# Optimization experiments

Hardware: AMD Instinct MI355X
Metric: run time of the kernel (lower is better)

## Reference

```python
import jax, jax.numpy as jnp
import numpy as np

B_, L_, D_ = 2, 4096, 1024
E_ = 2
DI = E_ * D_            # 2048
H_ = 16
HD_ = DI // H_          # 128
N_ = 128
K_ = 4                  # d_conv
CS_ = 256               # SSD chunk size
MC_ = 256               # Hebbian memory chunk size
ALPHA = 0.5             # memory_alpha (== write_alpha default)


def _silu(x):
    return x * jax.nn.sigmoid(x)


def _rmsnorm(x, w, eps=1e-6):
    return x * jax.lax.rsqrt(jnp.mean(x * x, axis=-1, keepdims=True) + eps) * w


def setup_inputs() -> dict:
    key = jax.random.key(0)
    ks = jax.random.split(key, 8)
    proj_dim = 2 * DI + 2 * H_ * N_ + H_
    n = lambda k, sh, sc: jax.random.normal(k, sh, jnp.float32) * sc
    return {
        "x": n(ks[0], (B_, L_, D_), 1.0),
        "norm_w": jnp.ones((D_,), jnp.float32),
        "w_in": n(ks[1], (proj_dim, D_), 0.02),
        "conv_w": n(ks[2], (DI, K_), 0.2),
        "conv_b": jnp.zeros((DI,), jnp.float32),
        "A_log": jnp.log(2.0 * jnp.ones((H_,), jnp.float32)),
        "dt_bias": jnp.zeros((H_,), jnp.float32),
        "D_skip": jnp.ones((DI,), jnp.float32),
        "w_out": n(ks[3], (D_, DI), 0.02),
        "w_write": n(ks[4], (D_, D_), 0.02),
        "w_read": n(ks[5], (D_, D_), 0.02),
        "decay": jnp.float32(4.6),
    }


def _forward(x, norm_w, w_in, conv_w, conv_b, A_log, dt_bias, D_skip,
             w_out, w_write, w_read, decay):
    B, L, D = x.shape
    residual = x
    xn = _rmsnorm(x, norm_w)

    # ---- SSDBlock ----
    proj = xn @ w_in.T  # (B,L,2*DI+2*H*N+H)
    val = proj[..., :DI]
    gate = proj[..., DI:2 * DI]
    Bp = proj[..., 2 * DI:2 * DI + H_ * N_].reshape(B, L, H_, N_)
    Cp = proj[..., 2 * DI + H_ * N_:2 * DI + 2 * H_ * N_].reshape(B, L, H_, N_)
    dt = jax.nn.softplus(proj[..., -H_:] + dt_bias)  # (B,L,H)

    # causal depthwise conv1d (kernel K_, groups=DI)
    vp = jnp.pad(val, ((0, 0), (K_ - 1, 0), (0, 0)))
    val = sum(conv_w[:, k] * vp[:, k:k + L, :] for k in range(K_)) + conv_b
    val = _silu(val).reshape(B, L, H_, HD_)

    ld = dt * (-jnp.exp(A_log))  # log decay (B,L,H)

    nc = L // CS_
    to_chunks = lambda a: jnp.moveaxis(a.reshape(B, nc, CS_, *a.shape[2:]), 1, 0)
    tril = jnp.tril(jnp.ones((CS_, CS_), bool))
    Dv = D_skip.reshape(1, H_, 1, HD_)

    def ssd_chunk(h, inp):
        v_c, b_c, c_c, ld_c = inp  # (B,CS,H,HD), (B,CS,H,N), (B,CS,H,N), (B,CS,H)
        cum = jnp.cumsum(ld_c, axis=1)            # (B,CS,H)
        cum_h = jnp.transpose(cum, (0, 2, 1))     # (B,H,CS)
        dd = cum_h[:, :, :, None] - cum_h[:, :, None, :]
        Lmat = jnp.where(tril, jnp.exp(dd), 0.0)
        M = jnp.einsum('blhn,bmhn->bhlm', c_c, b_c) * Lmat
        v_h = jnp.transpose(v_c, (0, 2, 1, 3))    # (B,H,CS,HD)
        Y = M @ v_h
        Y = Y + jnp.einsum('blhn,bhdn,blh->bhld', c_c, h, jnp.exp(cum))
        Y = Y + Dv * v_h
        h = jnp.exp(cum[:, -1])[:, :, None, None] * h + \
            jnp.einsum('blhd,blhn,blh->bhdn', v_c, b_c, jnp.exp(cum[:, -1:, :] - cum))
        return h, Y

    h0 = jnp.zeros((B, H_, HD_, N_), jnp.float32)
    _, Ys = jax.lax.scan(ssd_chunk, h0,
                         (to_chunks(val), to_chunks(Bp), to_chunks(Cp), to_chunks(ld)))
    # (nc,B,H,CS,HD) -> (B,L,DI)
    Y = jnp.transpose(Ys, (1, 0, 3, 2, 4)).reshape(B, L, DI)
    out = (Y * _silu(gate)) @ w_out.T  # (B,L,D)

    # ---- Hebbian memory (chunkwise) ----
    gamma = jax.nn.sigmoid(decay)
    lg = jnp.log(gamma)
    v = out @ w_write.T
    wk = jnp.pad(out[:, :-1], ((0, 0), (1, 0), (0, 0)))  # shifted write keys
    p = jnp.arange(MC_)
    diffs = jnp.maximum(p[:, None] - 1 - p[None, :], 0).astype(jnp.float32)
    causal = (p[:, None] > p[None, :]).astype(jnp.float32)
    Mmem = jnp.exp(diffs * lg) * causal
    gp = gamma ** p                    # read decay by position in chunk
    gw = gamma ** (MC_ - 1 - p)        # write decay to end of chunk
    nm = L // MC_
    tom = lambda a: jnp.moveaxis(a.reshape(B, nm, MC_, D), 1, 0)

    def mem_chunk(W, inp):
        rk_c, wk_c, v_c = inp  # (B,MC,D)
        inter = jnp.einsum('bde,bte->btd', W, rk_c) * gp[None, :, None]
        S = jnp.einsum('bie,bje->bij', rk_c, wk_c)
        intra = (S * Mmem) @ v_c
        W = gamma ** MC_ * W + jnp.einsum('btd,bte->bde', v_c * gw[None, :, None], wk_c)
        return W, inter + intra

    W0 = jnp.zeros((B, D, D), jnp.float32)
    _, reads = jax.lax.scan(mem_chunk, W0, (tom(out), tom(wk), tom(v)))
    reads = jnp.moveaxis(reads, 0, 1).reshape(B, L, D)
    out = out + ALPHA * (reads @ w_read.T)
    return residual + out


def reference(x, norm_w, w_in, conv_w, conv_b, A_log, dt_bias, D_skip,
              w_out, w_write, w_read, decay):
    return _forward(x, norm_w, w_in, conv_w, conv_b, A_log, dt_bias, D_skip,
                    w_out, w_write, w_read, decay)
```

## Files before the change

### kernel.cpp

```cpp
#include <hip/hip_runtime.h>
#include <hip/hip_bf16.h>

typedef __hip_bfloat16 bf16;
typedef __attribute__((ext_vector_type(8))) short short8;
typedef __attribute__((ext_vector_type(4))) float floatx4;

#define B_ 2
#define L_ 4096
#define D_ 1024
#define DI_ 2048
#define H_ 16
#define HD_ 128
#define N_ 128
#define CS_ 256
#define MC_ 256
#define NC_ 16
#define PROJ_ 8208

__device__ __forceinline__ float bf2f(short s) {
    return __uint_as_float(((unsigned)(unsigned short)s) << 16);
}

__device__ __forceinline__ void gl_lds16(const void* g, void* s) {
    __builtin_amdgcn_global_load_lds(
        (const __attribute__((address_space(1))) void*)g,
        (__attribute__((address_space(3))) void*)s, 16, 0, 0);
}

struct GemmP {
    const bf16* A; const bf16* Bt;
    float* C; bf16* CB; bf16* CB2; bf16* CB3;
    const float* add0; const float* add1; const bf16* add0b; const float* scr;
    long lda, ldb, ldc;
    int M, N, K, zinner;
    long a_zo, a_zi, b_zo, b_zi, c_zo, c_zi;
};

template<int EPI>
__global__ __launch_bounds__(256, 2) void gemm_bt(GemmP p)
{
    int NT = gridDim.x, MT = gridDim.y;
    long T = (long)NT * MT * gridDim.z;
    long flat = ((long)blockIdx.z * MT + blockIdx.y) * NT + blockIdx.x;
    int xcd = (int)(flat & 7);
    long q = flat >> 3;
    long Tq = T >> 3; int Tr = (int)(T & 7);
    long tile = (long)xcd * Tq + (long)(xcd < Tr ? xcd : Tr) + q;
    long per_z = (long)NT * MT;
    int z = (int)(tile / per_z);
    int t2 = (int)(tile - (long)z * per_z);
    int FG = NT >> 3;
    int g, width, within;
    if (t2 < FG * MT * 8) { g = t2 / (MT * 8); width = 8; within = t2 - g * MT * 8; }
    else                  { g = FG; width = NT - FG * 8; within = t2 - FG * MT * 8; }
    int m_outer = within / (8 * width);
    int hb = MT - m_outer * 8; if (hb > 8) hb = 8;
    int inner = within - m_outer * 8 * width;
    int n_in = inner / hb, m_in = inner - n_in * hb;
    int m0 = (m_outer * 8 + m_in) * 128;
    int n0 = (g * 8 + n_in) * 128;

    int zo = z / p.zinner, zi = z % p.zinner;
    const bf16* A  = p.A  + (long)zo * p.a_zo + (long)zi * p.a_zi;
    const bf16* Bt = p.Bt + (long)zo * p.b_zo + (long)zi * p.b_zi;
    long coff = (long)zo * p.c_zo + (long)zi * p.c_zi;

    __shared__ __align__(16) bf16 As[128 * 64];
    __shared__ __align__(16) bf16 Bs[128 * 64];

    int tid = threadIdx.x;
    int lane = tid & 63, wave = tid >> 6;
    int wm = (wave >> 1) * 64, wn = (wave & 1) * 64;
    int r16 = lane & 15, q8 = (lane >> 4) * 8;

    floatx4 zero4 = {0.f, 0.f, 0.f, 0.f};
    floatx4 acc[4][4];
#pragma unroll
    for (int i = 0; i < 4; i++)
#pragma unroll
        for (int j = 0; j < 4; j++) acc[i][j] = zero4;

    int lrow = lane >> 3;
    int lc = ((lane & 7) ^ lrow) * 8;
    int wrow = wave * 32;
    int rx = lane & 7;

    for (int k0 = 0; k0 < p.K; k0 += 64) {
#pragma unroll
        for (int t = 0; t < 4; t++) {
            int row = wrow + t * 8 + lrow;
            gl_lds16(A + (long)(m0 + row) * p.lda + k0 + lc, &As[(wrow + t * 8) * 64]);
            int bn = n0 + row; if (bn > p.N - 1) bn = p.N - 1;
            gl_lds16(Bt + (long)bn * p.ldb + k0 + lc, &Bs[(wrow + t * 8) * 64]);
        }
        __syncthreads();
#pragma unroll
        for (int ks = 0; ks < 64; ks += 32) {
            int lb = (ks >> 3) + (lane >> 4);
            int po = ((lb ^ rx) << 3);
            short8 af[4], bq[4];
#pragma unroll
            for (int i = 0; i < 4; i++)
                af[i] = *(const short8*)&As[(wm + i * 16 + r16) * 64 + po];
#pragma unroll
            for (int j = 0; j < 4; j++)
                bq[j] = *(const short8*)&Bs[(wn + j * 16 + r16) * 64 + po];
#pragma unroll
            for (int i = 0; i < 4; i++)
#pragma unroll
                for (int j = 0; j < 4; j++)
                    acc[i][j] = __builtin_amdgcn_mfma_f32_16x16x32_bf16(af[i], bq[j], acc[i][j], 0, 0, 0);
        }
        __syncthreads();
    }

    int rq = (lane >> 4) * 4;
#pragma unroll
    for (int i = 0; i < 4; i++) {
#pragma unroll
        for (int j = 0; j < 4; j++) {
#pragma unroll
            for (int r = 0; r < 4; r++) {
                int gm = m0 + wm + i * 16 + rq + r;
                int gn = n0 + wn + j * 16 + r16;
                if (gm >= p.M || gn >= p.N) continue;
                float a = acc[i][j][r];
                if (EPI == 0) {
                    p.C[coff + (long)gm * p.ldc + gn] = a;
                } else if (EPI == 2) {
                    if (gn < 2048)      p.CB [(long)gm * 2048 + gn]          = __float2bfloat16(a);
                    else if (gn < 4096) p.CB2[(long)gm * 2048 + (gn - 2048)] = __float2bfloat16(a);
                    else if (gn < 8192) p.CB3[(long)gm * 4096 + (gn - 4096)] = __float2bfloat16(a);
                    else                p.C  [(long)gm * 16   + (gn - 8192)] = a;
                } else if (EPI == 3) {
                    float lg = p.scr[1];
                    float v = (gm > gn) ? a * __expf((float)(gm - 1 - gn) * lg) : 0.f;
                    p.CB[coff + (long)gm * p.ldc + gn] = __float2bfloat16(v);
                } else if (EPI == 4) {
                    long ix = coff + (long)gm * p.ldc + gn;
                    float t = a * p.scr[16 + gm] + __bfloat162float(p.add0b[ix]);
                    p.CB[ix] = __float2bfloat16(t);
                } else if (EPI == 6) {
                    p.CB[coff + (long)gm * p.ldc + gn] = __float2bfloat16(a);
                } else if (EPI == 7) {
                    long ix = (long)gm * p.ldc + gn;
                    p.C[ix] = p.add0[ix] + __bfloat162float(p.add0b[ix]) + 0.5f * a;
                }
            }
        }
    }
}

__global__ void k_gamma(const float* decay, float* scr)
{
    int t = threadIdx.x;
    float g = 1.f / (1.f + expf(-decay[0]));
    float lg = logf(g);
    if (t == 0) { scr[0] = g; scr[1] = lg; scr[2] = expf(256.f * lg); }
    scr[16 + t]  = expf(lg * (float)t);
    scr[272 + t] = expf(lg * (float)(255 - t));
}

__global__ void k_f2ball(const float* __restrict__ s0, bf16* __restrict__ d0, long n0,
                         const float* __restrict__ s1, bf16* __restrict__ d1, long n1,
                         const float* __restrict__ s2, bf16* __restrict__ d2, long n2,
                         const float* __restrict__ s3, bf16* __restrict__ d3, long n3)
{
    long i = (long)blockIdx.x * 256 + threadIdx.x;
    const float* s; bf16* d; long rel = i;
    if (rel < n0) { s = s0; d = d0; }
    else { rel -= n0;
        if (rel < n1) { s = s1; d = d1; }
        else { rel -= n1;
            if (rel < n2) { s = s2; d = d2; }
            else { rel -= n2; if (rel >= n3) return; s = s3; d = d3; }
        }
    }
    float4 v = ((const float4*)s)[rel];
    bf16* o = d + rel * 4;
    o[0] = __float2bfloat16(v.x); o[1] = __float2bfloat16(v.y);
    o[2] = __float2bfloat16(v.z); o[3] = __float2bfloat16(v.w);
}

__global__ __launch_bounds__(256) void k_rmsnorm(const float* __restrict__ x,
                                                 const float* __restrict__ w,
                                                 bf16* __restrict__ o)
{
    int row = blockIdx.x, t = threadIdx.x;
    float4 xv = ((const float4*)(x + (long)row * D_))[t];
    float s = xv.x*xv.x + xv.y*xv.y + xv.z*xv.z + xv.w*xv.w;
#pragma unroll
    for (int m = 32; m > 0; m >>= 1) s += __shfl_xor(s, m, 64);
    __shared__ float ps[4];
    if ((t & 63) == 0) ps[t >> 6] = s;
    __syncthreads();
    s = ps[0] + ps[1] + ps[2] + ps[3];
    float r = rsqrtf(s * (1.f / (float)D_) + 1e-6f);
    float4 wv = ((const float4*)w)[t];
    bf16* orow = o + (long)row * D_ + t * 4;
    orow[0] = __float2bfloat16(xv.x * r * wv.x);
    orow[1] = __float2bfloat16(xv.y * r * wv.y);
    orow[2] = __float2bfloat16(xv.z * r * wv.z);
    orow[3] = __float2bfloat16(xv.w * r * wv.w);
}

__global__ __launch_bounds__(256) void k_cum(const float* __restrict__ dtr,
                                             const float* __restrict__ dt_bias,
                                             const float* __restrict__ A_log,
                                             float* __restrict__ cum_g,
                                             float* __restrict__ cumlast)
{
    int bid = blockIdx.x;
    int h = bid & 15, c = (bid >> 4) & 15, b = bid >> 8;
    long rowbase = (long)b * L_ + c * CS_;
    int tid = threadIdx.x;
    __shared__ float cum_s[256];
    float d = dtr[(rowbase + tid) * H_ + h] + dt_bias[h];
    float sp = (d > 20.f) ? d : log1pf(__expf(d));
    cum_s[tid] = -__expf(A_log[h]) * sp;
    __syncthreads();
    for (int off = 1; off < 256; off <<= 1) {
        float add = (tid >= off) ? cum_s[tid - off] : 0.f;
        __syncthreads();
        cum_s[tid] += add;
        __syncthreads();
    }
    cum_g[(rowbase + tid) * H_ + h] = cum_s[tid];
    if (tid == 255) cumlast[bid] = cum_s[255];
}

__global__ void k_vtc(const bf16* __restrict__ val_b, const float* __restrict__ cw,
                      const float* __restrict__ cb, bf16* __restrict__ vT)
{
    __shared__ bf16 tile[35][33];
    int b = blockIdx.z;
    int r0 = blockIdx.x * 32, c0 = blockIdx.y * 32;
    int tid = threadIdx.x;
    for (int idx = tid; idx < 35 * 32; idx += 256) {
        int row = idx >> 5, ch = idx & 31;
        int gl = r0 - 3 + row;
        bf16 v = __float2bfloat16(0.f);
        if (gl >= 0 && gl < L_) v = val_b[((long)b * L_ + gl) * 2048 + c0 + ch];
        tile[row][ch] = v;
    }
    __syncthreads();
    int tx = tid & 31, ty = tid >> 5;
    int l = r0 + tx;
    for (int i = 0; i < 32; i += 8) {
        int ch = c0 + ty + i;
        float4 cwv = ((const float4*)cw)[ch];
        float acc = cb[ch]
                  + cwv.x * __bfloat162float(tile[tx][ty + i])
                  + cwv.y * __bfloat162float(tile[tx + 1][ty + i])
                  + cwv.z * __bfloat162float(tile[tx + 2][ty + i])
                  + cwv.w * __bfloat162float(tile[tx + 3][ty + i]);
        float s = acc / (1.f + __expf(-acc));
        vT[((long)b * 2048 + ch) * L_ + l] = __float2bfloat16(s);
    }
}

__global__ void k_bt(const bf16* __restrict__ bc, bf16* __restrict__ BT)
{
    __shared__ bf16 tile[32][33];
    int b = blockIdx.z;
    int r0 = blockIdx.x * 32, c0 = blockIdx.y * 32;
    int tx = threadIdx.x & 31, ty = threadIdx.x >> 5;
    for (int i = 0; i < 32; i += 8)
        tile[ty + i][tx] = bc[((long)b * L_ + r0 + ty + i) * 4096 + c0 + tx];
    __syncthreads();
    int l = r0 + tx;
    for (int i = 0; i < 32; i += 8) {
        int col = c0 + ty + i;
        BT[((long)b * 2048 + col) * L_ + l] = tile[tx][ty + i];
    }
}

__global__ __launch_bounds__(256, 2) void k_ssd_u2(
    const bf16* __restrict__ vT, const bf16* __restrict__ BT,
    const float* __restrict__ cum_g, const float* __restrict__ cumlast,
    float* __restrict__ U)
{
    int bid = blockIdx.x;
    int h = bid & 15, c = (bid >> 4) & 15, b = bid >> 8;
    long rowbase = (long)b * L_ + c * CS_;
    int tid = threadIdx.x;
    __shared__ float w_s[256];
    w_s[tid] = __expf(cumlast[bid] - cum_g[(rowbase + tid) * H_ + h]);
    __syncthreads();
    int lane = tid & 63, wave = tid >> 6;
    int r16 = lane & 15, q8 = (lane >> 4) * 8, rq = (lane >> 4) * 4;
    int d0 = (wave >> 1) * 64, n0 = (wave & 1) * 64;
    const bf16* vb = vT + ((long)b * 2048 + h * 128) * L_ + c * 256;
    const bf16* bb = BT + ((long)b * 2048 + h * 128) * L_ + c * 256;
    floatx4 zero4 = {0.f, 0.f, 0.f, 0.f};
    floatx4 acc[4][4];
#pragma unroll
    for (int i = 0; i < 4; i++)
#pragma unroll
        for (int j = 0; j < 4; j++) acc[i][j] = zero4;
#pragma unroll 2
    for (int ks = 0; ks < 8; ks++) {
        float wv[8];
#pragma unroll
        for (int j = 0; j < 8; j++) wv[j] = w_s[ks * 32 + q8 + j];
        short8 af[4], bq[4];
#pragma unroll
        for (int i = 0; i < 4; i++) {
            short8 raw = *(const short8*)(vb + (long)(d0 + i * 16 + r16) * L_ + ks * 32 + q8);
#pragma unroll
            for (int j = 0; j < 8; j++) {
                float f = bf2f(raw[j]) * wv[j];
                raw[j] = (short)(__float_as_uint(f) >> 16);
            }
            af[i] = raw;
        }
#pragma unroll
        for (int j = 0; j < 4; j++)
            bq[j] = *(const short8*)(bb + (long)(n0 + j * 16 + r16) * L_ + ks * 32 + q8);
#pragma unroll
        for (int i = 0; i < 4; i++)
#pragma unroll
            for (int j = 0; j < 4; j++)
                acc[i][j] = __builtin_amdgcn_mfma_f32_16x16x32_bf16(af[i], bq[j], acc[i][j], 0, 0, 0);
    }
    float* up = U + (((long)c * B_ + b) * H_ + h) * 16384;
#pragma unroll
    for (int i = 0; i < 4; i++)
#pragma unroll
        for (int j = 0; j < 4; j++)
#pragma unroll
            for (int r = 0; r < 4; r++)
                up[(d0 + i * 16 + rq + r) * 128 + (n0 + j * 16 + r16)] = acc[i][j][r];
}

__global__ void k_ssd2(const float* __restrict__ U, const float* __restrict__ cumlast,
                       bf16* __restrict__ hst)
{
    long idx = (long)blockIdx.x * 256 + threadIdx.x;
    const long tot = (long)B_ * H_ * HD_ * N_;
    if (idx >= tot) return;
    int bh = (int)(idx >> 14);
    int b = bh >> 4, h = bh & 15;
    float hv = 0.f;
    for (int c = 0; c < NC_; c++) {
        hst[c * tot + idx] = __float2bfloat16(hv);
        float ef = __expf(cumlast[b * 256 + c * 16 + h]);
        hv = ef * hv + U[c * tot + idx];
    }
}

__global__ __launch_bounds__(256, 2) void k_ssd_y(
    const bf16* __restrict__ bc_b, const bf16* __restrict__ vT,
    const bf16* __restrict__ hst, const float* __restrict__ cum_g,
    const float* __restrict__ Dskip, const bf16* __restrict__ gate_b,
    bf16* __restrict__ yg)
{
    int bid = blockIdx.x;
    int h = bid & 15, c = (bid >> 4) & 15, b = bid >> 8;
    long rowbase = (long)b * L_ + c * CS_;
    int tid = threadIdx.x, lane = tid & 63, wave = tid >> 6;
    int r16 = lane & 15, q8 = (lane >> 4) * 8, rq = (lane >> 4) * 4;
    int wt = (wave >> 1) * 32, wmS = (wave & 1) * 32, wd = (wave & 1) * 64;

    __shared__ float cum_s[256];
    __shared__ __align__(16) bf16 Ss[64][72];

    cum_s[tid] = cum_g[(rowbase + tid) * H_ + h];
    __syncthreads();

    const bf16* Cb  = bc_b + rowbase * 4096 + 2048 + h * 128;
    const bf16* Bb  = bc_b + rowbase * 4096 + h * 128;
    const bf16* vTb = vT + ((long)b * 2048 + h * 128) * L_ + c * 256;
    const bf16* hp  = hst + (((long)c * B_ + b) * H_ + h) * 16384;

    floatx4 zero4 = {0.f, 0.f, 0.f, 0.f};

    for (int tt = 0; tt < 4; tt++) {
        int tbase = tt * 64;
        short8 caf[2][4];
#pragma unroll
        for (int i = 0; i < 2; i++)
#pragma unroll
            for (int ks = 0; ks < 4; ks++)
                caf[i][ks] = *(const short8*)(Cb + (long)(tbase + wt + i * 16 + r16) * 4096 + ks * 32 + q8);

        floatx4 yacc[2][4];
#pragma unroll
        for (int i = 0; i < 2; i++)
#pragma unroll
            for (int j = 0; j < 4; j++) yacc[i][j] = zero4;
#pragma unroll
        for (int ks = 0; ks < 4; ks++)
#pragma unroll
            for (int j = 0; j < 4; j++) {
                short8 hq = *(const short8*)(hp + (long)(wd + j * 16 + r16) * 128 + ks * 32 + q8);
#pragma unroll
                for (int i = 0; i < 2; i++)
                    yacc[i][j] = __builtin_amdgcn_mfma_f32_16x16x32_bf16(caf[i][ks], hq, yacc[i][j], 0, 0, 0);
            }
        float texp[2][4];
#pragma unroll
        for (int i = 0; i < 2; i++)
#pragma unroll
            for (int r = 0; r < 4; r++)
                texp[i][r] = __expf(cum_s[tbase + wt + i * 16 + rq + r]);
#pragma unroll
        for (int i = 0; i < 2; i++)
#pragma unroll
            for (int j = 0; j < 4; j++)
#pragma unroll
                for (int r = 0; r < 4; r++) yacc[i][j][r] *= texp[i][r];

        for (int mt = 0; mt <= tt; mt++) {
            int mbase = mt * 64;
            floatx4 sacc[2][2];
#pragma unroll
            for (int i = 0; i < 2; i++)
#pragma unroll
                for (int j = 0; j < 2; j++) sacc[i][j] = zero4;
#pragma unroll
            for (int ks = 0; ks < 4; ks++) {
                short8 bq[2];
#pragma unroll
                for (int j = 0; j < 2; j++)
                    bq[j] = *(const short8*)(Bb + (long)(mbase + wmS + j * 16 + r16) * 4096 + ks * 32 + q8);
#pragma unroll
                for (int i = 0; i < 2; i++)
#pragma unroll
                    for (int j = 0; j < 2; j++)
                        sacc[i][j] = __builtin_amdgcn_mfma_f32_16x16x32_bf16(caf[i][ks], bq[j], sacc[i][j], 0, 0, 0);
            }
            __syncthreads();
#pragma unroll
            for (int i = 0; i < 2; i++)
#pragma unroll
                for (int r = 0; r < 4; r++) {
                    int trow = wt + i * 16 + rq + r;
                    float ct = cum_s[tbase + trow];
#pragma unroll
                    for (int j = 0; j < 2; j++) {
                        int mcol = mbase + wmS + j * 16 + r16;
                        float val = (mcol <= tbase + trow) ? sacc[i][j][r] * __expf(ct - cum_s[mcol]) : 0.f;
                        Ss[trow][wmS + j * 16 + r16] = __float2bfloat16(val);
                    }
                }
            __syncthreads();
#pragma unroll
            for (int ks = 0; ks < 2; ks++) {
                short8 saf[2];
#pragma unroll
                for (int i = 0; i < 2; i++)
                    saf[i] = *(const short8*)&Ss[wt + i * 16 + r16][ks * 32 + q8];
#pragma unroll
                for (int j = 0; j < 4; j++) {
                    short8 vq = *(const short8*)(vTb + (long)(wd + j * 16 + r16) * L_ + mbase + ks * 32 + q8);
#pragma unroll
                    for (int i = 0; i < 2; i++)
                        yacc[i][j] = __builtin_amdgcn_mfma_f32_16x16x32_bf16(saf[i], vq, yacc[i][j], 0, 0, 0);
                }
            }
        }
#pragma unroll
        for (int i = 0; i < 2; i++)
#pragma unroll
            for (int r = 0; r < 4; r++) {
                int t = tbase + wt + i * 16 + rq + r;
                long grow = (rowbase + t) * 2048 + h * 128;
#pragma unroll
                for (int j = 0; j < 4; j++) {
                    int d = wd + j * 16 + r16;
                    float vv = __bfloat162float(vTb[(long)d * L_ + t]);
                    float y = yacc[i][j][r] + Dskip[h * 128 + d] * vv;
                    float g = __bfloat162float(gate_b[grow + d]);
                    float sg = g / (1.f + __expf(-g));
                    yg[grow + d] = __float2bfloat16(y * sg);
                }
            }
    }
}

__global__ void k_shift(const bf16* __restrict__ ob, bf16* __restrict__ wk)
{
    long idx = (long)blockIdx.x * 256 + threadIdx.x;
    if (idx >= (long)B_ * L_ * D_) return;
    int l = (int)((idx >> 10) & (L_ - 1));
    wk[idx] = (l == 0) ? __float2bfloat16(0.f) : ob[idx - D_];
}

__global__ void k_transpose_b(const bf16* __restrict__ srcg, bf16* __restrict__ dstg)
{
    __shared__ bf16 t[32][33];
    int b = blockIdx.z;
    const bf16* src = srcg + (long)b * L_ * D_;
    bf16* dst = dstg + (long)b * D_ * L_;
    int r0 = blockIdx.x * 32, c0 = blockIdx.y * 32;
    int tx = threadIdx.x & 31, ty = threadIdx.x >> 5;
    for (int i = 0; i < 32; i += 8)
        t[ty + i][tx] = src[(long)(r0 + ty + i) * D_ + c0 + tx];
    __syncthreads();
    for (int i = 0; i < 32; i += 8)
        dst[(long)(c0 + ty + i) * L_ + r0 + tx] = t[tx][ty + i];
}

__global__ void k_trans_wkg(const bf16* __restrict__ outg, const float* __restrict__ scr,
                            bf16* __restrict__ dstg)
{
    __shared__ float t[32][33];
    int b = blockIdx.z;
    const bf16* src = outg + (long)b * L_ * D_;
    bf16* dst = dstg + (long)b * D_ * L_;
    int r0 = blockIdx.x * 32, c0 = blockIdx.y * 32;
    int tx = threadIdx.x & 31, ty = threadIdx.x >> 5;
    for (int i = 0; i < 32; i += 8) {
        int rr = r0 + ty + i;
        float g = scr[272 + (rr & 255)];
        t[ty + i][tx] = (rr == 0) ? 0.f : __bfloat162float(src[(long)(rr - 1) * D_ + c0 + tx]) * g;
    }
    __syncthreads();
    for (int i = 0; i < 32; i += 8)
        dst[(long)(c0 + ty + i) * L_ + r0 + tx] = __float2bfloat16(t[tx][ty + i]);
}

__global__ void k_m2(bf16* __restrict__ UwW, const float* __restrict__ scr)
{
    long idx = (long)blockIdx.x * 256 + threadIdx.x;
    const long tot = (long)B_ * D_ * D_;
    if (idx >= tot) return;
    float gMC = scr[2];
    float w = 0.f;
    for (int c = 0; c < NC_; c++) {
        float tmp = __bfloat162float(UwW[c * tot + idx]);
        UwW[c * tot + idx] = __float2bfloat16(w);
        w = gMC * w + tmp;
    }
}

static inline int cdiv_i(long a, long b) { return (int)((a + b - 1) / b); }

static void run_gemm(hipStream_t st, int epi, const bf16* A, const bf16* Bt,
                     float* C, bf16* CB, bf16* CB2, bf16* CB3,
                     const float* add0, const float* add1, const bf16* add0b,
                     const float* scr, int M, int N, int K,
                     long lda, long ldb, long ldc, int nbatch, int zinner,
                     long a_zo, long a_zi, long b_zo, long b_zi, long c_zo, long c_zi)
{
    GemmP p;
    p.A = A; p.Bt = Bt; p.C = C; p.CB = CB; p.CB2 = CB2; p.CB3 = CB3;
    p.add0 = add0; p.add1 = add1; p.add0b = add0b; p.scr = scr;
    p.lda = lda; p.ldb = ldb; p.ldc = ldc;
    p.M = M; p.N = N; p.K = K; p.zinner = zinner;
    p.a_zo = a_zo; p.a_zi = a_zi; p.b_zo = b_zo; p.b_zi = b_zi; p.c_zo = c_zo; p.c_zi = c_zi;
    dim3 g(cdiv_i(N, 128), cdiv_i(M, 128), nbatch);
    dim3 b(256);
    switch (epi) {
        case 0: gemm_bt<0><<<g, b, 0, st>>>(p); break;
        case 2: gemm_bt<2><<<g, b, 0, st>>>(p); break;
        case 3: gemm_bt<3><<<g, b, 0, st>>>(p); break;
        case 4: gemm_bt<4><<<g, b, 0, st>>>(p); break;
        case 6: gemm_bt<6><<<g, b, 0, st>>>(p); break;
        case 7: gemm_bt<7><<<g, b, 0, st>>>(p); break;
    }
}

extern "C" void kernel_launch(void* const* d_in, const int* in_sizes, int n_in,
                              void* d_out, int out_size, void* d_ws, size_t ws_size,
                              hipStream_t stream)
{
    const float* x       = (const float*)d_in[0];
    const float* norm_w  = (const float*)d_in[1];
    const float* w_in    = (const float*)d_in[2];
    const float* conv_w  = (const float*)d_in[3];
    const float* conv_b  = (const float*)d_in[4];
    const float* A_log   = (const float*)d_in[5];
    const float* dt_bias = (const float*)d_in[6];
    const float* D_skip  = (const float*)d_in[7];
    const float* w_out   = (const float*)d_in[8];
    const float* w_write = (const float*)d_in[9];
    const float* w_read  = (const float*)d_in[10];
    const float* decay   = (const float*)d_in[11];
    float* outp = (float*)d_out;

    const size_t SZ_SCR  = 4096;
    const size_t SZ_DT   = (size_t)B_ * L_ * H_ * 4;
    const size_t SZ_CUML = 2048;
    const size_t SZ_WOUT = (size_t)D_ * DI_ * 2;
    const size_t SZ_WSML = (size_t)D_ * D_ * 2;
    const size_t SZ_R1   = (size_t)B_ * L_ * 2048 * 2;
    const size_t SZ_R2   = SZ_R1;
    const size_t SZ_R3   = (size_t)B_ * L_ * 4096 * 2;
    const size_t SZ_R4   = (size_t)B_ * L_ * D_ * 2 + (size_t)PROJ_ * D_ * 2;
    const size_t SZ_R5   = (size_t)B_ * L_ * 2048 * 4;

    size_t o = 0;
    auto take = [&](size_t sz) { size_t r = o; o += (sz + 255) & ~(size_t)255; return r; };
    const size_t O_SCR = take(SZ_SCR);
    const size_t O_DT  = take(SZ_DT);
    const size_t O_LD  = take(SZ_DT);
    const size_t O_CUM = take(SZ_DT);
    const size_t O_CL  = take(SZ_CUML);
    const size_t O_WO  = take(SZ_WOUT);
    const size_t O_WW  = take(SZ_WSML);
    const size_t O_WR  = take(SZ_WSML);
    const size_t O_R1  = take(SZ_R1);
    const size_t O_R2  = take(SZ_R2);
    const size_t O_R3  = take(SZ_R3);
    const size_t O_R4  = take(SZ_R4);
    const size_t O_R5  = take(SZ_R5);
    const size_t NEED = o;
    if (ws_size < NEED) return;
    (void)O_LD;

    char* ws = (char*)d_ws;
    float* scr     = (float*)(ws + O_SCR);
    float* dt_raw  = (float*)(ws + O_DT);
    float* cum_g   = (float*)(ws + O_CUM);
    float* cumlast = (float*)(ws + O_CL);
    bf16*  w_out_b   = (bf16*)(ws + O_WO);
    bf16*  w_write_b = (bf16*)(ws + O_WW);
    bf16*  w_read_b  = (bf16*)(ws + O_WR);

    bf16*  val_b   = (bf16*)(ws + O_R1);
    bf16*  yg_b    = (bf16*)(ws + O_R1);
    bf16*  hst_b   = (bf16*)(ws + O_R1 + (size_t)B_ * L_ * D_ * 2);
    bf16*  Sm_b    = (bf16*)(ws + O_R1);
    bf16*  intra_b = (bf16*)(ws + O_R1 + (size_t)NC_ * B_ * MC_ * MC_ * 2);
    bf16*  gate_b  = (bf16*)(ws + O_R2);
    bf16*  out_b   = (bf16*)(ws + O_R2);
    bf16*  wk_b    = (bf16*)(ws + O_R2 + (size_t)B_ * L_ * D_ * 2);
    bf16*  reads_b = wk_b;
    bf16*  bc_b    = (bf16*)(ws + O_R3);
    bf16*  UwW     = (bf16*)(ws + O_R3);
    bf16*  xn_b    = (bf16*)(ws + O_R4);
    bf16*  w_in_b  = (bf16*)(ws + O_R4 + (size_t)B_ * L_ * D_ * 2);
    float* U_ssd   = (float*)(ws + O_R4);
    bf16*  vT_g    = (bf16*)(ws + O_R5);
    bf16*  BT_g    = (bf16*)(ws + O_R5 + (size_t)B_ * L_ * 2048 * 2);
    bf16*  vbuf_b  = (bf16*)(ws + O_R5);
    bf16*  vTm     = (bf16*)(ws + O_R5 + (size_t)B_ * L_ * D_ * 4);
    bf16*  wkgT    = (bf16*)(ws + O_R5 + (size_t)B_ * L_ * D_ * 4 + (size_t)B_ * L_ * D_ * 2);

    const long BLD = (long)B_ * L_ * D_;

    k_gamma<<<1, 256, 0, stream>>>(decay, scr);
    {
        long n0 = (long)PROJ_ * D_ / 4, n1 = (long)D_ * DI_ / 4;
        long n2 = (long)D_ * D_ / 4,   n3 = n2;
        k_f2ball<<<cdiv_i(n0 + n1 + n2 + n3, 256), 256, 0, stream>>>(
            w_in, w_in_b, n0, w_out, w_out_b, n1, w_write, w_write_b, n2, w_read, w_read_b, n3);
    }
    k_rmsnorm<<<B_ * L_, 256, 0, stream>>>(x, norm_w, xn_b);
    run_gemm(stream, 2, xn_b, w_in_b, dt_raw, val_b, gate_b, bc_b, nullptr, nullptr, nullptr, nullptr,
             B_ * L_, PROJ_, D_, D_, D_, 0, 1, 1, 0, 0, 0, 0, 0, 0);
    k_cum<<<B_ * NC_ * H_, 256, 0, stream>>>(dt_raw, dt_bias, A_log, cum_g, cumlast);
    k_vtc<<<dim3(L_ / 32, DI_ / 32, B_), 256, 0, stream>>>(val_b, conv_w, conv_b, vT_g);
    k_bt<<<dim3(L_ / 32, DI_ / 32, B_), 256, 0, stream>>>(bc_b, BT_g);
    k_ssd_u2<<<B_ * NC_ * H_, 256, 0, stream>>>(vT_g, BT_g, cum_g, cumlast, U_ssd);
    k_ssd2<<<cdiv_i((long)B_ * H_ * HD_ * N_, 256), 256, 0, stream>>>(U_ssd, cumlast, hst_b);
    k_ssd_y<<<B_ * NC_ * H_, 256, 0, stream>>>(bc_b, vT_g, hst_b, cum_g, D_skip, gate_b, yg_b);
    run_gemm(stream, 6, yg_b, w_out_b, nullptr, out_b, nullptr, nullptr, nullptr, nullptr, nullptr, nullptr,
             B_ * L_, D_, DI_, DI_, DI_, D_, 1, 1, 0, 0, 0, 0, 0, 0);
    k_shift<<<cdiv_i(BLD, 256), 256, 0, stream>>>(out_b, wk_b);
    run_gemm(stream, 6, out_b, w_write_b, nullptr, vbuf_b, nullptr, nullptr, nullptr, nullptr, nullptr, nullptr,
             B_ * L_, D_, D_, D_, D_, D_, 1, 1, 0, 0, 0, 0, 0, 0);
    k_transpose_b<<<dim3(L_ / 32, D_ / 32, B_), 256, 0, stream>>>(vbuf_b, vTm);
    k_trans_wkg<<<dim3(L_ / 32, D_ / 32, B_), 256, 0, stream>>>(out_b, scr, wkgT);
    run_gemm(stream, 6, vTm, wkgT, nullptr, UwW, nullptr, nullptr, nullptr, nullptr, nullptr, nullptr,
             D_, D_, MC_, L_, L_, D_, B_ * NC_, NC_,
             (long)D_ * L_, MC_, (long)D_ * L_, MC_, (long)D_ * D_, (long)B_ * D_ * D_);
    k_m2<<<cdiv_i((long)B_ * D_ * D_, 256), 256, 0, stream>>>(UwW, scr);
    run_gemm(stream, 3, out_b, wk_b, nullptr, Sm_b, nullptr, nullptr, nullptr, nullptr, nullptr, scr,
             MC_, MC_, D_, D_, D_, MC_, B_ * NC_, NC_,
             (long)L_ * D_, (long)MC_ * D_, (long)L_ * D_, (long)MC_ * D_,
             (long)MC_ * MC_, (long)B_ * MC_ * MC_);
    run_gemm(stream, 6, Sm_b, vTm, nullptr, intra_b, nullptr, nullptr, nullptr, nullptr, nullptr, nullptr,
             MC_, D_, MC_, MC_, L_, D_, B_ * NC_, NC_,
             (long)MC_ * MC_, (long)B_ * MC_ * MC_, (long)D_ * L_, MC_,
             (long)L_ * D_, (long)MC_ * D_);
    run_gemm(stream, 4, out_b, UwW, nullptr, reads_b, nullptr, nullptr, nullptr, nullptr, intra_b, scr,
             MC_, D_, D_, D_, D_, D_, B_ * NC_, NC_,
             (long)L_ * D_, (long)MC_ * D_, (long)D_ * D_, (long)B_ * D_ * D_,
             (long)L_ * D_, (long)MC_ * D_);
    run_gemm(stream, 7, reads_b, w_read_b, outp, nullptr, nullptr, nullptr, x, nullptr, out_b, nullptr,
             B_ * L_, D_, D_, D_, D_, D_, 1, 1, 0, 0, 0, 0, 0, 0);
}
```

Before: 813.5 us.

## Switch GEMM to 32x32x16 MFMA and fuse shift into out-proj epilogue

The shared GEMM kernel now uses 32x32x16 bf16 MFMA tiles with 16-wide accumulators instead of 16x16x32. This cuts the number of LDS fragment loads per MFMA and changes the accumulator layout, so the epilogue index mapping is rewritten to match. Separately, the standalone k_shift kernel is removed. The output-projection GEMM now writes the one-row-shifted copy (wk) directly in a new epilogue 8, saving a full read and write pass over the activation and one launch.

Result: faster. 748.5 us (-8.0%).

```diff
diff --git a/kernel.cpp b/kernel.cpp
--- a/kernel.cpp
+++ b/kernel.cpp
@@ -4,6 +4,7 @@
 typedef __hip_bfloat16 bf16;
 typedef __attribute__((ext_vector_type(8))) short short8;
 typedef __attribute__((ext_vector_type(4))) float floatx4;
+typedef __attribute__((ext_vector_type(16))) float floatx16;
 
 #define B_ 2
 #define L_ 4096
@@ -71,14 +72,15 @@
     int tid = threadIdx.x;
     int lane = tid & 63, wave = tid >> 6;
     int wm = (wave >> 1) * 64, wn = (wave & 1) * 64;
-    int r16 = lane & 15, q8 = (lane >> 4) * 8;
-
-    floatx4 zero4 = {0.f, 0.f, 0.f, 0.f};
-    floatx4 acc[4][4];
-#pragma unroll
-    for (int i = 0; i < 4; i++)
-#pragma unroll
-        for (int j = 0; j < 4; j++) acc[i][j] = zero4;
+    int ln31 = lane & 31, hi = lane >> 5;
+
+    floatx16 acc[2][2];
+#pragma unroll
+    for (int i = 0; i < 2; i++)
+#pragma unroll
+        for (int j = 0; j < 2; j++)
+#pragma unroll
+            for (int r = 0; r < 16; r++) acc[i][j][r] = 0.f;
 
     int lrow = lane >> 3;
     int lc = ((lane & 7) ^ lrow) * 8;
@@ -95,34 +97,33 @@
         }
         __syncthreads();
 #pragma unroll
-        for (int ks = 0; ks < 64; ks += 32) {
-            int lb = (ks >> 3) + (lane >> 4);
+        for (int ks = 0; ks < 64; ks += 16) {
+            int lb = (ks >> 3) + hi;
             int po = ((lb ^ rx) << 3);
-            short8 af[4], bq[4];
-#pragma unroll
-            for (int i = 0; i < 4; i++)
-                af[i] = *(const short8*)&As[(wm + i * 16 + r16) * 64 + po];
-#pragma unroll
-            for (int j = 0; j < 4; j++)
-                bq[j] = *(const short8*)&Bs[(wn + j * 16 + r16) * 64 + po];
-#pragma unroll
-            for (int i = 0; i < 4; i++)
-#pragma unroll
-                for (int j = 0; j < 4; j++)
-                    acc[i][j] = __builtin_amdgcn_mfma_f32_16x16x32_bf16(af[i], bq[j], acc[i][j], 0, 0, 0);
+            short8 af[2], bq[2];
+#pragma unroll
+            for (int i = 0; i < 2; i++)
+                af[i] = *(const short8*)&As[(wm + i * 32 + ln31) * 64 + po];
+#pragma unroll
+            for (int j = 0; j < 2; j++)
+                bq[j] = *(const short8*)&Bs[(wn + j * 32 + ln31) * 64 + po];
+#pragma unroll
+            for (int i = 0; i < 2; i++)
+#pragma unroll
+                for (int j = 0; j < 2; j++)
+                    acc[i][j] = __builtin_amdgcn_mfma_f32_32x32x16_bf16(af[i], bq[j], acc[i][j], 0, 0, 0);
         }
         __syncthreads();
     }
 
-    int rq = (lane >> 4) * 4;
-#pragma unroll
-    for (int i = 0; i < 4; i++) {
-#pragma unroll
-        for (int j = 0; j < 4; j++) {
-#pragma unroll
-            for (int r = 0; r < 4; r++) {
-                int gm = m0 + wm + i * 16 + rq + r;
-                int gn = n0 + wn + j * 16 + r16;
+#pragma unroll
+    for (int i = 0; i < 2; i++) {
+#pragma unroll
+        for (int j = 0; j < 2; j++) {
+#pragma unroll
+            for (int r = 0; r < 16; r++) {
+                int gm = m0 + wm + i * 32 + (r & 3) + 8 * (r >> 2) + 4 * hi;
+                int gn = n0 + wn + j * 32 + ln31;
                 if (gm >= p.M || gn >= p.N) continue;
                 float a = acc[i][j][r];
                 if (EPI == 0) {
@@ -145,6 +146,13 @@
                 } else if (EPI == 7) {
                     long ix = (long)gm * p.ldc + gn;
                     p.C[ix] = p.add0[ix] + __bfloat162float(p.add0b[ix]) + 0.5f * a;
+                } else if (EPI == 8) {
+                    long ix = (long)gm * p.ldc + gn;
+                    bf16 v = __float2bfloat16(a);
+                    p.CB[ix] = v;
+                    int l = gm & (L_ - 1);
+                    if (l != L_ - 1) p.CB2[ix + p.ldc] = v;
+                    if (l == 0) p.CB2[ix] = __float2bfloat16(0.f);
                 }
             }
         }
@@ -477,14 +485,6 @@
                 }
             }
     }
-}
-
-__global__ void k_shift(const bf16* __restrict__ ob, bf16* __restrict__ wk)
-{
-    long idx = (long)blockIdx.x * 256 + threadIdx.x;
-    if (idx >= (long)B_ * L_ * D_) return;
-    int l = (int)((idx >> 10) & (L_ - 1));
-    wk[idx] = (l == 0) ? __float2bfloat16(0.f) : ob[idx - D_];
 }
 
 __global__ void k_transpose_b(const bf16* __restrict__ srcg, bf16* __restrict__ dstg)
@@ -559,6 +559,7 @@
         case 4: gemm_bt<4><<<g, b, 0, st>>>(p); break;
         case 6: gemm_bt<6><<<g, b, 0, st>>>(p); break;
         case 7: gemm_bt<7><<<g, b, 0, st>>>(p); break;
+        case 8: gemm_bt<8><<<g, b, 0, st>>>(p); break;
     }
 }
 
@@ -639,8 +640,6 @@
     bf16*  vTm     = (bf16*)(ws + O_R5 + (size_t)B_ * L_ * D_ * 4);
     bf16*  wkgT    = (bf16*)(ws + O_R5 + (size_t)B_ * L_ * D_ * 4 + (size_t)B_ * L_ * D_ * 2);
 
-    const long BLD = (long)B_ * L_ * D_;
-
     k_gamma<<<1, 256, 0, stream>>>(decay, scr);
     {
         long n0 = (long)PROJ_ * D_ / 4, n1 = (long)D_ * DI_ / 4;
@@ -657,9 +656,8 @@
     k_ssd_u2<<<B_ * NC_ * H_, 256, 0, stream>>>(vT_g, BT_g, cum_g, cumlast, U_ssd);
     k_ssd2<<<cdiv_i((long)B_ * H_ * HD_ * N_, 256), 256, 0, stream>>>(U_ssd, cumlast, hst_b);
     k_ssd_y<<<B_ * NC_ * H_, 256, 0, stream>>>(bc_b, vT_g, hst_b, cum_g, D_skip, gate_b, yg_b);
-    run_gemm(stream, 6, yg_b, w_out_b, nullptr, out_b, nullptr, nullptr, nullptr, nullptr, nullptr, nullptr,
+    run_gemm(stream, 8, yg_b, w_out_b, nullptr, out_b, wk_b, nullptr, nullptr, nullptr, nullptr, nullptr,
              B_ * L_, D_, DI_, DI_, DI_, D_, 1, 1, 0, 0, 0, 0, 0, 0);
-    k_shift<<<cdiv_i(BLD, 256), 256, 0, stream>>>(out_b, wk_b);
     run_gemm(stream, 6, out_b, w_write_b, nullptr, vbuf_b, nullptr, nullptr, nullptr, nullptr, nullptr, nullptr,
              B_ * L_, D_, D_, D_, D_, D_, 1, 1, 0, 0, 0, 0, 0, 0);
     k_transpose_b<<<dim3(L_ / 32, D_ / 32, B_), 256, 0, stream>>>(vbuf_b, vTm);
```
